# Optimization experiments

Hardware: AMD Instinct MI355X
Metric: run time of the kernel (lower is better)

The kernel has to match this reference:

```python
import jax, jax.numpy as jnp
import numpy as np

E, B, L, D = 3, 4, 1024, 768
DS = 64            # d_state
DI = 2 * D         # d_inner (expand=2)
DTR = 48           # dt_rank = ceil(D/16)
K = 4              # depthwise conv kernel size


def setup_inputs() -> dict:
    key = jax.random.key(0)
    ks = jax.random.split(key, 10)
    s = lambda i, shape, scale=0.02: (jax.random.normal(ks[i], shape, jnp.float32) * scale)
    A_log = jnp.broadcast_to(jnp.log(jnp.arange(1, DS + 1, dtype=jnp.float32)), (E, DI, DS))
    return {
        "base":   jax.random.normal(ks[0], (B, L, D), jnp.float32),
        "per_ch": jax.random.normal(ks[1], (E, B, L, D), jnp.float32),
        "alpha":  jnp.ones((E,), jnp.float32) / E,
        "ln_g":   jnp.ones((D,), jnp.float32),
        "ln_b":   jnp.zeros((D,), jnp.float32),
        "W_in":   s(2, (E, D, 2 * DI)),
        "conv_w": s(3, (E, DI, K), 0.1),
        "conv_b": jnp.zeros((E, DI), jnp.float32),
        "W_x":    s(4, (E, DI, DTR + 2 * DS)),
        "W_dt":   s(5, (E, DTR, DI), 0.05),
        "b_dt":   jnp.full((E, DI), -4.6, jnp.float32),  # softplus^-1(~0.01)
        "A_log":  A_log,
        "D_skip": jnp.ones((E, DI), jnp.float32),
        "W_out":  s(6, (E, DI, D)),
    }


def layer_norm(x, g, b, eps=1e-5):
    mu = jnp.mean(x, axis=-1, keepdims=True)
    var = jnp.mean(jnp.square(x - mu), axis=-1, keepdims=True)
    return (x - mu) * jax.lax.rsqrt(var + eps) * g + b


def mamba(x, W_in, conv_w, conv_b, W_x, W_dt, b_dt, A_log, D_skip, W_out):
    # x: [B, L, D]
    xz = x @ W_in                                   # [B, L, 2*DI]
    xp, z = jnp.split(xz, 2, axis=-1)               # each [B, L, DI]
    # causal depthwise conv along L
    xc = jnp.pad(xp, ((0, 0), (K - 1, 0), (0, 0)))
    xc = jax.lax.conv_general_dilated(
        jnp.swapaxes(xc, 1, 2),                     # [B, DI, L+K-1]
        conv_w[:, None, :],                         # [DI, 1, K]
        window_strides=(1,), padding='VALID',
        dimension_numbers=('NCH', 'OIH', 'NCH'),
        feature_group_count=DI)
    xc = jnp.swapaxes(xc, 1, 2) + conv_b            # [B, L, DI]
    xs = jax.nn.silu(xc)
    dbl = xs @ W_x                                  # [B, L, DTR+2*DS]
    dt, Bm, Cm = jnp.split(dbl, [DTR, DTR + DS], axis=-1)
    dt = jax.nn.softplus(dt @ W_dt + b_dt)          # [B, L, DI]
    A = -jnp.exp(A_log)                             # [DI, DS]

    def step(h, t):
        u_t, dt_t, B_t, C_t = t                     # [B,DI],[B,DI],[B,DS],[B,DS]
        dA = jnp.exp(dt_t[..., None] * A)           # [B, DI, DS]
        h = dA * h + (dt_t * u_t)[..., None] * B_t[:, None, :]
        y = jnp.einsum('bds,bs->bd', h, C_t)
        return h, y

    tm = lambda a: jnp.swapaxes(a, 0, 1)            # time-major
    h0 = jnp.zeros((x.shape[0], DI, DS), x.dtype)
    _, ys = jax.lax.scan(step, h0, (tm(xs), tm(dt), tm(Bm), tm(Cm)))
    y = jnp.swapaxes(ys, 0, 1) + xs * D_skip        # [B, L, DI]
    y = y * jax.nn.silu(z)
    return y @ W_out                                # [B, L, D]


def reference(base, per_ch, alpha, ln_g, ln_b, W_in, conv_w, conv_b, W_x,
              W_dt, b_dt, A_log, D_skip, W_out):
    w = jax.nn.softmax(alpha)                       # [E]
    xn = layer_norm(per_ch, ln_g, ln_b)             # shared LN on each channel
    outs = jax.vmap(mamba)(xn, W_in, conv_w, conv_b, W_x,
                           W_dt, b_dt, A_log, D_skip, W_out)  # [E, B, L, D]
    injection = jnp.einsum('e,ebld->bld', w, outs)
    return base + injection
```

## Files before the change

### kernel.cpp

```cpp
#include <hip/hip_runtime.h>
#include <hip/hip_bf16.h>

typedef __hip_bfloat16 bf16;
typedef unsigned short u16;
typedef __attribute__((ext_vector_type(8))) short s16x8;
typedef __attribute__((ext_vector_type(4))) short s16x4;
typedef __attribute__((ext_vector_type(4))) float f32x4;

#define EXP 3
#define BB  4
#define LL  1024
#define DD  768
#define DSN 64
#define DIN 1536
#define DTR 48
#define MM  4096

struct alignas(8)  bf16x4 { bf16 v[4]; };
struct alignas(16) bf16x8 { bf16 v[8]; };

__device__ __forceinline__ float siluf(float x) { return x / (1.f + __expf(-x)); }
__device__ __forceinline__ float softplusf(float x) { return (x > 15.f) ? x : log1pf(__expf(x)); }
__device__ __forceinline__ float bf2f(u16 h) { union { unsigned u; float f; } x; x.u = ((unsigned)h) << 16; return x.f; }

template <int CTRL>
__device__ __forceinline__ float ror_add(float x) {
  int y = __builtin_amdgcn_update_dpp(0, __float_as_int(x), CTRL, 0xf, 0xf, true);
  return x + __int_as_float(y);
}

__launch_bounds__(256)
__global__ void ln_apply_k(const float* __restrict__ pc, const float* __restrict__ lng,
                           const float* __restrict__ lnb, bf16* __restrict__ out) {
  int row  = blockIdx.x * 4 + (threadIdx.x >> 6);
  int lane = threadIdx.x & 63;
  const float* x = pc + (size_t)row * DD;
  float4 v[3];
  float s = 0.f, sq = 0.f;
#pragma unroll
  for (int i = 0; i < 3; i++) {
    v[i] = *(const float4*)(x + lane * 4 + i * 256);
    s  += v[i].x + v[i].y + v[i].z + v[i].w;
    sq += v[i].x * v[i].x + v[i].y * v[i].y + v[i].z * v[i].z + v[i].w * v[i].w;
  }
#pragma unroll
  for (int o = 1; o < 64; o <<= 1) { s += __shfl_xor(s, o); sq += __shfl_xor(sq, o); }
  float mu = s * (1.f / 768.f);
  float rs = rsqrtf(sq * (1.f / 768.f) - mu * mu + 1e-5f);
  bf16* op = out + (size_t)row * DD;
#pragma unroll
  for (int i = 0; i < 3; i++) {
    int col = lane * 4 + i * 256;
    float4 g4 = *(const float4*)(lng + col);
    float4 b4 = *(const float4*)(lnb + col);
    bf16x4 pk;
    pk.v[0] = (bf16)((v[i].x - mu) * rs * g4.x + b4.x);
    pk.v[1] = (bf16)((v[i].y - mu) * rs * g4.y + b4.y);
    pk.v[2] = (bf16)((v[i].z - mu) * rs * g4.z + b4.z);
    pk.v[3] = (bf16)((v[i].w - mu) * rs * g4.w + b4.w);
    *(bf16x4*)(op + col) = pk;
  }
}

__launch_bounds__(256)
__global__ void tcvt_k(const float* __restrict__ in, bf16* __restrict__ out,
                       int Ksrc, int ldin, int ldout,
                       size_t sIn, size_t sOut, int mode, const float* __restrict__ alphap) {
  __shared__ float tl[32][33];
  int z = blockIdx.z;
  const float* src = in + (size_t)z * sIn;
  bf16* dst = out + (size_t)z * sOut;
  int n0 = blockIdx.x * 32, k0 = blockIdx.y * 32;
  int tx = threadIdx.x, ty = threadIdx.y;
  int n = n0 + tx;
  int c = n; bool nv = true;
  if (mode == 1) {
    if (n < 48)       c = n;
    else if (n < 64)  nv = false;
    else if (n < 192) c = n - 16;
    else              nv = false;
  }
  float scale = 1.f;
  if (mode == 2) {
    float a0 = alphap[0], a1 = alphap[1], a2 = alphap[2];
    float mx = fmaxf(a0, fmaxf(a1, a2));
    float e0 = __expf(a0 - mx), e1 = __expf(a1 - mx), e2 = __expf(a2 - mx);
    scale = ((z == 0) ? e0 : (z == 1) ? e1 : e2) / (e0 + e1 + e2);
  }
#pragma unroll
  for (int i = 0; i < 32; i += 8) {
    int k = k0 + ty + i;
    float v = (nv && k < Ksrc) ? src[(size_t)k * ldin + c] : 0.f;
    tl[ty + i][tx] = v * scale;
  }
  __syncthreads();
#pragma unroll
  for (int i = 0; i < 32; i += 8) {
    dst[(size_t)(n0 + ty + i) * ldout + (k0 + tx)] = (bf16)tl[tx][ty + i];
  }
}

__launch_bounds__(256)
__global__ void conv_silu_k(const bf16* __restrict__ xp, const float* __restrict__ cw,
                            const float* __restrict__ cb, bf16* __restrict__ xs) {
  long i = ((long)blockIdx.x * 256 + threadIdx.x) * 8;
  int  c  = (int)(i % DIN);
  long rl = i / DIN;
  int  l  = (int)(rl & (LL - 1));
  int  e  = (int)(rl >> 12);
  const float* wp  = cw + (size_t)e * DIN * 4 + (size_t)c * 4;
  const float* cbp = cb + (size_t)e * DIN + c;
  float acc[8];
#pragma unroll
  for (int j = 0; j < 8; j++) acc[j] = cbp[j];
#pragma unroll
  for (int tap = 0; tap < 4; tap++) {
    if (l - 3 + tap >= 0) {
      s16x8 xv = *(const s16x8*)(const void*)(xp + (rl + tap - 3) * DIN + c);
#pragma unroll
      for (int j = 0; j < 8; j++)
        acc[j] = fmaf(bf2f((u16)xv[j]), wp[j * 4 + tap], acc[j]);
    }
  }
  bf16x8 pk;
#pragma unroll
  for (int j = 0; j < 8; j++) pk.v[j] = (bf16)siluf(acc[j]);
  *(bf16x8*)(xs + rl * DIN + c) = pk;
}

template<int MODE>
__launch_bounds__(256)
__global__ void mfma_gemm_k(const bf16* __restrict__ A, const bf16* __restrict__ Bt,
                            int Kdim, int lda,
                            size_t sA, size_t sB, size_t sO,
                            bf16* __restrict__ o0, bf16* __restrict__ o1,
                            const float* __restrict__ bias,
                            float* __restrict__ outp) {
  __shared__ short As[128 * 32];
  __shared__ short Bs[128 * 32];
  int z = blockIdx.z;
  A  += (size_t)z * sA;
  Bt += (size_t)z * sB;
  if (o0) o0 += (size_t)z * sO;
  if (o1) o1 += (size_t)z * sO;
  if constexpr (MODE == 1) outp += (size_t)z * (size_t)MM * 128;
  const float* bz = (MODE == 2) ? bias + (size_t)z * DIN : bias;

  int t = threadIdx.x;
  int l = t & 63, w = t >> 6;
  int wr = w >> 1, wc = w & 1;
  int n0 = blockIdx.x * 128, r0 = blockIdx.y * 128;

  int row = t >> 2, c3 = t & 3, col = c3 * 8;
  int plo = ((c3 & 1) ? 16 : 0) + ((c3 & 2) ? 4 : 0);
  int lrow = (l & 15) * 32 + (l >> 4) * 8;

  f32x4 acc[4][4] = {};

  for (int k0 = 0; k0 < Kdim; k0 += 32) {
    s16x8 va0 = *(const s16x8*)(const void*)(A  + (size_t)(r0 + row)      * lda  + k0 + col);
    s16x8 va1 = *(const s16x8*)(const void*)(A  + (size_t)(r0 + row + 64) * lda  + k0 + col);
    s16x8 vb0 = *(const s16x8*)(const void*)(Bt + (size_t)(n0 + row)      * Kdim + k0 + col);
    s16x8 vb1 = *(const s16x8*)(const void*)(Bt + (size_t)(n0 + row + 64) * Kdim + k0 + col);
    __syncthreads();
    *(s16x4*)(As + row * 32 + plo)          = __builtin_shufflevector(va0, va0, 0, 1, 2, 3);
    *(s16x4*)(As + row * 32 + plo + 8)      = __builtin_shufflevector(va0, va0, 4, 5, 6, 7);
    *(s16x4*)(As + (row + 64) * 32 + plo)     = __builtin_shufflevector(va1, va1, 0, 1, 2, 3);
    *(s16x4*)(As + (row + 64) * 32 + plo + 8) = __builtin_shufflevector(va1, va1, 4, 5, 6, 7);
    *(s16x4*)(Bs + row * 32 + plo)          = __builtin_shufflevector(vb0, vb0, 0, 1, 2, 3);
    *(s16x4*)(Bs + row * 32 + plo + 8)      = __builtin_shufflevector(vb0, vb0, 4, 5, 6, 7);
    *(s16x4*)(Bs + (row + 64) * 32 + plo)     = __builtin_shufflevector(vb1, vb1, 0, 1, 2, 3);
    *(s16x4*)(Bs + (row + 64) * 32 + plo + 8) = __builtin_shufflevector(vb1, vb1, 4, 5, 6, 7);
    __syncthreads();
    s16x8 af[4], bfv[4];
#pragma unroll
    for (int m = 0; m < 4; m++) af[m]  = *(const s16x8*)(As + (wr * 64 + m * 16) * 32 + lrow);
#pragma unroll
    for (int n = 0; n < 4; n++) bfv[n] = *(const s16x8*)(Bs + (wc * 64 + n * 16) * 32 + lrow);
#pragma unroll
    for (int m = 0; m < 4; m++)
#pragma unroll
      for (int n = 0; n < 4; n++)
        acc[m][n] = __builtin_amdgcn_mfma_f32_16x16x32_bf16(af[m], bfv[n], acc[m][n], 0, 0, 0);
  }

  int rb = r0 + wr * 64 + ((l >> 4) << 2);
  int cb = n0 + wc * 64 + (l & 15);
#pragma unroll
  for (int m = 0; m < 4; m++)
#pragma unroll
    for (int n = 0; n < 4; n++)
#pragma unroll
      for (int r = 0; r < 4; r++) {
        int gr = rb + m * 16 + r;
        int gc = cb + n * 16;
        float v = acc[m][n][r];
        if constexpr (MODE == 0) {
          if (n0 < DIN) o0[(size_t)gr * DIN + gc] = (bf16)v;
          else          o1[(size_t)gr * DIN + (gc - DIN)] = (bf16)siluf(v);
        } else if constexpr (MODE == 1) {
          if (gc < 64)       o0[(size_t)gr * 64 + gc] = (bf16)v;
          else if (gc < 192) outp[(size_t)gr * 128 + (gc - 64)] = v;
        } else if constexpr (MODE == 2) {
          o0[(size_t)gr * DIN + gc] = (bf16)softplusf(v + bz[gc]);
        } else {
          atomicAdd(&outp[(size_t)gr * DD + gc], v);
        }
      }
}

__launch_bounds__(256)
__global__ void copy4_k(const float* __restrict__ s, float* __restrict__ d, int n4) {
  int i = blockIdx.x * 256 + threadIdx.x;
  if (i < n4) ((float4*)d)[i] = ((const float4*)s)[i];
}

__launch_bounds__(256)
__global__ void scan_k(const bf16* __restrict__ dtb, bf16* __restrict__ xsb,
                       const bf16* __restrict__ gb, const float* __restrict__ dbl,
                       const float* __restrict__ A_log, const float* __restrict__ Dsk) {
  int gt = blockIdx.x * 256 + threadIdx.x;
  int sg = gt & 15;
  int cidx = gt >> 4;
  int d  = cidx % DIN;
  int eb = cidx / DIN;
  int e  = eb >> 2;

  float4 Ar = *(const float4*)(A_log + ((size_t)e * DIN + d) * DSN + sg * 4);
  const float LOG2E = 1.44269504088896f;
  float4 A2;
  A2.x = -__expf(Ar.x) * LOG2E;
  A2.y = -__expf(Ar.y) * LOG2E;
  A2.z = -__expf(Ar.z) * LOG2E;
  A2.w = -__expf(Ar.w) * LOG2E;
  float4 h = {0.f, 0.f, 0.f, 0.f};
  float dskip = Dsk[(size_t)e * DIN + d];

  unsigned idx  = (unsigned)eb * (LL * DIN) + (unsigned)d;
  unsigned bofs = (unsigned)eb * (LL * 128) + (unsigned)(sg * 4);

  float dtv = (float)dtb[idx];
  float u   = (float)xsb[idx];
  float gv  = (float)gb[idx];
  float4 Bv = *(const float4*)(dbl + bofs);
  float4 Cv = *(const float4*)(dbl + bofs + 64);

#pragma unroll 4
  for (int l = 0; l < LL; ++l) {
    unsigned idxn = idx + DIN;
    unsigned bofn = bofs + 128;
    float dtn = (float)dtb[idxn];
    float un  = (float)xsb[idxn];
    float gn  = (float)gb[idxn];
    float4 Bn = *(const float4*)(dbl + bofn);
    float4 Cn = *(const float4*)(dbl + bofn + 64);

    float du = dtv * u;
    float4 dA;
    dA.x = __builtin_amdgcn_exp2f(dtv * A2.x);
    dA.y = __builtin_amdgcn_exp2f(dtv * A2.y);
    dA.z = __builtin_amdgcn_exp2f(dtv * A2.z);
    dA.w = __builtin_amdgcn_exp2f(dtv * A2.w);
    h.x = fmaf(dA.x, h.x, du * Bv.x);
    h.y = fmaf(dA.y, h.y, du * Bv.y);
    h.z = fmaf(dA.z, h.z, du * Bv.z);
    h.w = fmaf(dA.w, h.w, du * Bv.w);
    float p = fmaf(h.x, Cv.x, fmaf(h.y, Cv.y, fmaf(h.z, Cv.z, h.w * Cv.w)));
    p = ror_add<0x128>(p);
    p = ror_add<0x124>(p);
    p = ror_add<0x122>(p);
    p = ror_add<0x121>(p);
    if (sg == 0) {
      xsb[idx] = (bf16)(fmaf(u, dskip, p) * gv);
    }
    idx = idxn; bofs = bofn;
    dtv = dtn; u = un; gv = gn; Bv = Bn; Cv = Cn;
  }
}

extern "C" void kernel_launch(void* const* d_in, const int* in_sizes, int n_in,
                              void* d_out, int out_size, void* d_ws, size_t ws_size,
                              hipStream_t stream) {
  const float* base   = (const float*)d_in[0];
  const float* per_ch = (const float*)d_in[1];
  const float* alpha  = (const float*)d_in[2];
  const float* ln_g   = (const float*)d_in[3];
  const float* ln_b   = (const float*)d_in[4];
  const float* W_in   = (const float*)d_in[5];
  const float* conv_w = (const float*)d_in[6];
  const float* conv_b = (const float*)d_in[7];
  const float* W_x    = (const float*)d_in[8];
  const float* W_dt   = (const float*)d_in[9];
  const float* b_dt   = (const float*)d_in[10];
  const float* A_log  = (const float*)d_in[11];
  const float* D_skip = (const float*)d_in[12];
  const float* W_out  = (const float*)d_in[13];
  float* out = (float*)d_out;
  (void)in_sizes; (void)n_in; (void)out_size; (void)ws_size;

  char* ws = (char*)d_ws;
  const size_t R = (size_t)EXP * MM * DIN * 2;
  bf16* Abf   = (bf16*)ws;
  bf16* xsws  = (bf16*)ws;
  bf16* gws   = (bf16*)(ws + R);
  bf16* dtws  = (bf16*)(ws + 2 * R);
  char* R4    = ws + 3 * R;
  bf16*  WinT  = (bf16*)R4;
  bf16*  WoutT = (bf16*)R4;
  float* dblf  = (float*)(R4 + 7077888);
  bf16* WxT   = (bf16*)(ws + 3 * R + 14155776);
  bf16* WdtT  = (bf16*)(ws + 3 * R + 14155776 + 2359296);
  bf16* dblp  = (bf16*)(ws + 3 * R + 14155776 + 2359296 + 589824);

  dim3 blk2(32, 8);

  ln_apply_k<<<EXP * BB * LL / 4, 256, 0, stream>>>(per_ch, ln_g, ln_b, Abf);
  tcvt_k<<<dim3(96, 24, EXP), blk2, 0, stream>>>(W_in, WinT, 768, 3072, 768,
        (size_t)768 * 3072, (size_t)3072 * 768, 0, nullptr);
  tcvt_k<<<dim3(8, 48, EXP), blk2, 0, stream>>>(W_x, WxT, 1536, 176, 1536,
        (size_t)1536 * 176, (size_t)256 * 1536, 1, nullptr);
  tcvt_k<<<dim3(48, 2, EXP), blk2, 0, stream>>>(W_dt, WdtT, 48, 1536, 64,
        (size_t)48 * 1536, (size_t)1536 * 64, 0, nullptr);

  mfma_gemm_k<0><<<dim3(24, 32, EXP), 256, 0, stream>>>(Abf, WinT, 768, DD,
        (size_t)MM * DD, (size_t)3072 * 768, (size_t)MM * DIN,
        dtws, gws, nullptr, nullptr);

  tcvt_k<<<dim3(24, 48, EXP), blk2, 0, stream>>>(W_out, WoutT, 1536, 768, 1536,
        (size_t)1536 * 768, (size_t)768 * 1536, 2, alpha);

  conv_silu_k<<<EXP * BB * LL * DIN / 8 / 256, 256, 0, stream>>>(dtws, conv_w, conv_b, xsws);

  mfma_gemm_k<1><<<dim3(2, 32, EXP), 256, 0, stream>>>(xsws, WxT, 1536, DIN,
        (size_t)MM * DIN, (size_t)256 * 1536, (size_t)MM * 64,
        dblp, nullptr, nullptr, dblf);

  mfma_gemm_k<2><<<dim3(12, 32, EXP), 256, 0, stream>>>(dblp, WdtT, 64, 64,
        (size_t)MM * 64, (size_t)1536 * 64, (size_t)MM * DIN,
        dtws, nullptr, b_dt, nullptr);

  copy4_k<<<MM * DD / 4 / 256, 256, 0, stream>>>(base, out, MM * DD / 4);
  scan_k<<<EXP * BB * DIN * 16 / 256, 256, 0, stream>>>(dtws, xsws, gws, dblf, A_log, D_skip);
  mfma_gemm_k<3><<<dim3(6, 32, EXP), 256, 0, stream>>>(xsws, WoutT, 1536, DIN,
        (size_t)MM * DIN, (size_t)768 * 1536, 0,
        nullptr, nullptr, nullptr, out);
}
```

Before: 898.3 us.

## Store dt and B/C time-major-transposed so scan loads contiguous vectors per channel

The dt projection GEMM now computes the transposed product so dt is stored as [E, DI, B*L], and the x-projection GEMM writes B/C as [E, 128, B*L] with vector stores. The scan reads four timesteps of dt in one 8-byte load and four timesteps of B/C per float4, then processes four steps per loop iteration. This replaces strided per-step loads of dt and B/C with contiguous vector loads and adds more prefetching per iteration. In exchange the MODE 1 epilogue performs transposed stores, and the scan holds more registers, which may lower occupancy.

```diff
diff --git a/kernel.cpp b/kernel.cpp
--- a/kernel.cpp
+++ b/kernel.cpp
@@ -143,7 +143,7 @@
   Bt += (size_t)z * sB;
   if (o0) o0 += (size_t)z * sO;
   if (o1) o1 += (size_t)z * sO;
-  if constexpr (MODE == 1) outp += (size_t)z * (size_t)MM * 128;
+  if constexpr (MODE == 1) outp += (size_t)z * (size_t)128 * MM;
   const float* bz = (MODE == 2) ? bias + (size_t)z * DIN : bias;
 
   int t = threadIdx.x;
@@ -186,27 +186,42 @@
 
   int rb = r0 + wr * 64 + ((l >> 4) << 2);
   int cb = n0 + wc * 64 + (l & 15);
-#pragma unroll
-  for (int m = 0; m < 4; m++)
-#pragma unroll
-    for (int n = 0; n < 4; n++)
-#pragma unroll
-      for (int r = 0; r < 4; r++) {
-        int gr = rb + m * 16 + r;
-        int gc = cb + n * 16;
-        float v = acc[m][n][r];
-        if constexpr (MODE == 0) {
-          if (n0 < DIN) o0[(size_t)gr * DIN + gc] = (bf16)v;
-          else          o1[(size_t)gr * DIN + (gc - DIN)] = (bf16)siluf(v);
-        } else if constexpr (MODE == 1) {
-          if (gc < 64)       o0[(size_t)gr * 64 + gc] = (bf16)v;
-          else if (gc < 192) outp[(size_t)gr * 128 + (gc - 64)] = v;
-        } else if constexpr (MODE == 2) {
-          o0[(size_t)gr * DIN + gc] = (bf16)softplusf(v + bz[gc]);
-        } else {
-          atomicAdd(&outp[(size_t)gr * DD + gc], v);
+
+  if constexpr (MODE == 1) {
+#pragma unroll
+    for (int m = 0; m < 4; m++)
+#pragma unroll
+      for (int n = 0; n < 4; n++) {
+        int gr0 = rb + m * 16;
+        int gc  = cb + n * 16;
+        if (gc < 64) {
+#pragma unroll
+          for (int r = 0; r < 4; r++)
+            o0[(size_t)(gr0 + r) * 64 + gc] = (bf16)acc[m][n][r];
+        } else if (gc < 192) {
+          *(f32x4*)(outp + (size_t)(gc - 64) * MM + gr0) = acc[m][n];
         }
       }
+  } else {
+#pragma unroll
+    for (int m = 0; m < 4; m++)
+#pragma unroll
+      for (int n = 0; n < 4; n++)
+#pragma unroll
+        for (int r = 0; r < 4; r++) {
+          int gr = rb + m * 16 + r;
+          int gc = cb + n * 16;
+          float v = acc[m][n][r];
+          if constexpr (MODE == 0) {
+            if (n0 < DIN) o0[(size_t)gr * DIN + gc] = (bf16)v;
+            else          o1[(size_t)gr * DIN + (gc - DIN)] = (bf16)siluf(v);
+          } else if constexpr (MODE == 2) {
+            o0[(size_t)gr * MM + gc] = (bf16)softplusf(v + bz[gr]);
+          } else {
+            atomicAdd(&outp[(size_t)gr * DD + gc], v);
+          }
+        }
+  }
 }
 
 __launch_bounds__(256)
@@ -216,66 +231,89 @@
 }
 
 __launch_bounds__(256)
-__global__ void scan_k(const bf16* __restrict__ dtb, bf16* __restrict__ xsb,
-                       const bf16* __restrict__ gb, const float* __restrict__ dbl,
+__global__ void scan_k(const bf16* __restrict__ dtT, bf16* __restrict__ xsb,
+                       const bf16* __restrict__ gb, const float* __restrict__ bcT,
                        const float* __restrict__ A_log, const float* __restrict__ Dsk) {
   int gt = blockIdx.x * 256 + threadIdx.x;
   int sg = gt & 15;
   int cidx = gt >> 4;
   int d  = cidx % DIN;
   int eb = cidx / DIN;
-  int e  = eb >> 2;
+  int e  = eb >> 2, b = eb & 3;
 
   float4 Ar = *(const float4*)(A_log + ((size_t)e * DIN + d) * DSN + sg * 4);
   const float LOG2E = 1.44269504088896f;
-  float4 A2;
-  A2.x = -__expf(Ar.x) * LOG2E;
-  A2.y = -__expf(Ar.y) * LOG2E;
-  A2.z = -__expf(Ar.z) * LOG2E;
-  A2.w = -__expf(Ar.w) * LOG2E;
-  float4 h = {0.f, 0.f, 0.f, 0.f};
+  float A2x = -__expf(Ar.x) * LOG2E;
+  float A2y = -__expf(Ar.y) * LOG2E;
+  float A2z = -__expf(Ar.z) * LOG2E;
+  float A2w = -__expf(Ar.w) * LOG2E;
   float dskip = Dsk[(size_t)e * DIN + d];
 
-  unsigned idx  = (unsigned)eb * (LL * DIN) + (unsigned)d;
-  unsigned bofs = (unsigned)eb * (LL * 128) + (unsigned)(sg * 4);
-
-  float dtv = (float)dtb[idx];
-  float u   = (float)xsb[idx];
-  float gv  = (float)gb[idx];
-  float4 Bv = *(const float4*)(dbl + bofs);
-  float4 Cv = *(const float4*)(dbl + bofs + 64);
-
-#pragma unroll 4
-  for (int l = 0; l < LL; ++l) {
-    unsigned idxn = idx + DIN;
-    unsigned bofn = bofs + 128;
-    float dtn = (float)dtb[idxn];
-    float un  = (float)xsb[idxn];
-    float gn  = (float)gb[idxn];
-    float4 Bn = *(const float4*)(dbl + bofn);
-    float4 Cn = *(const float4*)(dbl + bofn + 64);
-
-    float du = dtv * u;
-    float4 dA;
-    dA.x = __builtin_amdgcn_exp2f(dtv * A2.x);
-    dA.y = __builtin_amdgcn_exp2f(dtv * A2.y);
-    dA.z = __builtin_amdgcn_exp2f(dtv * A2.z);
-    dA.w = __builtin_amdgcn_exp2f(dtv * A2.w);
-    h.x = fmaf(dA.x, h.x, du * Bv.x);
-    h.y = fmaf(dA.y, h.y, du * Bv.y);
-    h.z = fmaf(dA.z, h.z, du * Bv.z);
-    h.w = fmaf(dA.w, h.w, du * Bv.w);
-    float p = fmaf(h.x, Cv.x, fmaf(h.y, Cv.y, fmaf(h.z, Cv.z, h.w * Cv.w)));
-    p = ror_add<0x128>(p);
-    p = ror_add<0x124>(p);
-    p = ror_add<0x122>(p);
-    p = ror_add<0x121>(p);
-    if (sg == 0) {
-      xsb[idx] = (bf16)(fmaf(u, dskip, p) * gv);
-    }
-    idx = idxn; bofs = bofn;
-    dtv = dtn; u = un; gv = gn; Bv = Bn; Cv = Cn;
-  }
+  const uint2*  dtp = (const uint2*)(dtT + (((size_t)e * DIN + d) << 12) + (b << 10));
+  const float4* Bq  = (const float4*)(bcT + (((size_t)e * 128 + sg * 4) << 12) + (b << 10));
+  unsigned idx = (unsigned)eb * (LL * DIN) + (unsigned)d;
+
+  float hx = 0.f, hy = 0.f, hz = 0.f, hw = 0.f;
+
+  uint2  dtu = dtp[0];
+  float4 B0 = Bq[0],     B1 = Bq[1024],  B2 = Bq[2048],  B3 = Bq[3072];
+  float4 C0 = Bq[65536], C1 = Bq[66560], C2 = Bq[67584], C3 = Bq[68608];
+  float u0 = (float)xsb[idx];
+  float u1 = (float)xsb[idx + DIN];
+  float u2 = (float)xsb[idx + 2 * DIN];
+  float u3 = (float)xsb[idx + 3 * DIN];
+  float g0 = (float)gb[idx];
+  float g1 = (float)gb[idx + DIN];
+  float g2 = (float)gb[idx + 2 * DIN];
+  float g3 = (float)gb[idx + 3 * DIN];
+
+#define SSTEP(DT, UU, GV, BX, BY, BZ, BW, CX, CY, CZ, CW, OFS)             \
+  {                                                                        \
+    float du = (DT) * (UU);                                                \
+    hx = fmaf(__builtin_amdgcn_exp2f((DT) * A2x), hx, du * (BX));          \
+    hy = fmaf(__builtin_amdgcn_exp2f((DT) * A2y), hy, du * (BY));          \
+    hz = fmaf(__builtin_amdgcn_exp2f((DT) * A2z), hz, du * (BZ));          \
+    hw = fmaf(__builtin_amdgcn_exp2f((DT) * A2w), hw, du * (BW));          \
+    float p = fmaf(hx, (CX), fmaf(hy, (CY), fmaf(hz, (CZ), hw * (CW))));   \
+    p = ror_add<0x128>(p);                                                 \
+    p = ror_add<0x124>(p);                                                 \
+    p = ror_add<0x122>(p);                                                 \
+    p = ror_add<0x121>(p);                                                 \
+    if (sg == 0) xsb[idx + (OFS)] = (bf16)(fmaf((UU), dskip, p) * (GV));   \
+  }
+
+  for (int t = 0; t < 256; ++t) {
+    uint2  dtn = dtp[t + 1];
+    float4 Bn0 = Bq[t + 1],     Bn1 = Bq[t + 1025],  Bn2 = Bq[t + 2049],  Bn3 = Bq[t + 3073];
+    float4 Cn0 = Bq[t + 65537], Cn1 = Bq[t + 66561], Cn2 = Bq[t + 67585], Cn3 = Bq[t + 68609];
+    unsigned idx4 = idx + 4 * DIN;
+    float un0 = (float)xsb[idx4];
+    float un1 = (float)xsb[idx4 + DIN];
+    float un2 = (float)xsb[idx4 + 2 * DIN];
+    float un3 = (float)xsb[idx4 + 3 * DIN];
+    float gn0 = (float)gb[idx4];
+    float gn1 = (float)gb[idx4 + DIN];
+    float gn2 = (float)gb[idx4 + 2 * DIN];
+    float gn3 = (float)gb[idx4 + 3 * DIN];
+
+    float dt0 = __uint_as_float(dtu.x << 16);
+    float dt1 = __uint_as_float(dtu.x & 0xffff0000u);
+    float dt2 = __uint_as_float(dtu.y << 16);
+    float dt3 = __uint_as_float(dtu.y & 0xffff0000u);
+
+    SSTEP(dt0, u0, g0, B0.x, B1.x, B2.x, B3.x, C0.x, C1.x, C2.x, C3.x, 0)
+    SSTEP(dt1, u1, g1, B0.y, B1.y, B2.y, B3.y, C0.y, C1.y, C2.y, C3.y, DIN)
+    SSTEP(dt2, u2, g2, B0.z, B1.z, B2.z, B3.z, C0.z, C1.z, C2.z, C3.z, 2 * DIN)
+    SSTEP(dt3, u3, g3, B0.w, B1.w, B2.w, B3.w, C0.w, C1.w, C2.w, C3.w, 3 * DIN)
+
+    idx = idx4;
+    dtu = dtn;
+    B0 = Bn0; B1 = Bn1; B2 = Bn2; B3 = Bn3;
+    C0 = Cn0; C1 = Cn1; C2 = Cn2; C3 = Cn3;
+    u0 = un0; u1 = un1; u2 = un2; u3 = un3;
+    g0 = gn0; g1 = gn1; g2 = gn2; g3 = gn3;
+  }
+#undef SSTEP
 }
 
 extern "C" void kernel_launch(void* const* d_in, const int* in_sizes, int n_in,
@@ -303,11 +341,12 @@
   bf16* Abf   = (bf16*)ws;
   bf16* xsws  = (bf16*)ws;
   bf16* gws   = (bf16*)(ws + R);
-  bf16* dtws  = (bf16*)(ws + 2 * R);
+  bf16* xpws  = (bf16*)(ws + 2 * R);
+  bf16* dtT   = (bf16*)(ws + 2 * R);
   char* R4    = ws + 3 * R;
   bf16*  WinT  = (bf16*)R4;
   bf16*  WoutT = (bf16*)R4;
-  float* dblf  = (float*)(R4 + 7077888);
+  float* bcT   = (float*)(R4 + 7077888);
   bf16* WxT   = (bf16*)(ws + 3 * R + 14155776);
   bf16* WdtT  = (bf16*)(ws + 3 * R + 14155776 + 2359296);
   bf16* dblp  = (bf16*)(ws + 3 * R + 14155776 + 2359296 + 589824);
@@ -324,23 +363,23 @@
 
   mfma_gemm_k<0><<<dim3(24, 32, EXP), 256, 0, stream>>>(Abf, WinT, 768, DD,
         (size_t)MM * DD, (size_t)3072 * 768, (size_t)MM * DIN,
-        dtws, gws, nullptr, nullptr);
+        xpws, gws, nullptr, nullptr);
 
   tcvt_k<<<dim3(24, 48, EXP), blk2, 0, stream>>>(W_out, WoutT, 1536, 768, 1536,
         (size_t)1536 * 768, (size_t)768 * 1536, 2, alpha);
 
-  conv_silu_k<<<EXP * BB * LL * DIN / 8 / 256, 256, 0, stream>>>(dtws, conv_w, conv_b, xsws);
+  conv_silu_k<<<EXP * BB * LL * DIN / 8 / 256, 256, 0, stream>>>(xpws, conv_w, conv_b, xsws);
 
   mfma_gemm_k<1><<<dim3(2, 32, EXP), 256, 0, stream>>>(xsws, WxT, 1536, DIN,
         (size_t)MM * DIN, (size_t)256 * 1536, (size_t)MM * 64,
-        dblp, nullptr, nullptr, dblf);
-
-  mfma_gemm_k<2><<<dim3(12, 32, EXP), 256, 0, stream>>>(dblp, WdtT, 64, 64,
-        (size_t)MM * 64, (size_t)1536 * 64, (size_t)MM * DIN,
-        dtws, nullptr, b_dt, nullptr);
+        dblp, nullptr, nullptr, bcT);
+
+  mfma_gemm_k<2><<<dim3(32, 12, EXP), 256, 0, stream>>>(WdtT, dblp, 64, 64,
+        (size_t)DIN * 64, (size_t)MM * 64, (size_t)DIN * MM,
+        dtT, nullptr, b_dt, nullptr);
 
   copy4_k<<<MM * DD / 4 / 256, 256, 0, stream>>>(base, out, MM * DD / 4);
-  scan_k<<<EXP * BB * DIN * 16 / 256, 256, 0, stream>>>(dtws, xsws, gws, dblf, A_log, D_skip);
+  scan_k<<<EXP * BB * DIN * 16 / 256, 256, 0, stream>>>(dtT, xsws, gws, bcT, A_log, D_skip);
   mfma_gemm_k<3><<<dim3(6, 32, EXP), 256, 0, stream>>>(xsws, WoutT, 1536, DIN,
         (size_t)MM * DIN, (size_t)768 * 1536, 0,
         nullptr, nullptr, nullptr, out);
```

After: 1.778 ms. 97.9% more time.

## Double-buffer MFMA GEMM tiles with direct global-to-LDS async loads

Applied to the files above, without the earlier changes.

The bf16 MFMA GEMM now stages A and B tiles straight from global memory into shared memory with `global_load_lds`, instead of loading into registers and shuffling stores. Shared memory is double-buffered so the next K-slice is fetched while MFMAs run on the current one, leaving one barrier per iteration. The LDS layout becomes two half-K planes, and fragments are rebuilt from two 4-element reads. This aims to hide global latency and drop register staging, at the cost of twice the LDS per block and reliance on correct wait handling for the async copies.

```diff
diff --git a/kernel.cpp b/kernel.cpp
--- a/kernel.cpp
+++ b/kernel.cpp
@@ -136,8 +136,8 @@
                             bf16* __restrict__ o0, bf16* __restrict__ o1,
                             const float* __restrict__ bias,
                             float* __restrict__ outp) {
-  __shared__ short As[128 * 32];
-  __shared__ short Bs[128 * 32];
+  __shared__ short As[2 * 128 * 32];
+  __shared__ short Bs[2 * 128 * 32];
   int z = blockIdx.z;
   A  += (size_t)z * sA;
   Bt += (size_t)z * sB;
@@ -151,38 +151,68 @@
   int wr = w >> 1, wc = w & 1;
   int n0 = blockIdx.x * 128, r0 = blockIdx.y * 128;
 
-  int row = t >> 2, c3 = t & 3, col = c3 * 8;
-  int plo = ((c3 & 1) ? 16 : 0) + ((c3 & 2) ? 4 : 0);
-  int lrow = (l & 15) * 32 + (l >> 4) * 8;
+  int s0  = w * 64 + l;
+  int rS  = (s0 >> 1) & 127;
+  int k8S = s0 & 1;
+  const bf16* srcA0 = A  + (size_t)(r0 + rS) * lda  + k8S * 8;
+  const bf16* srcA1 = srcA0 + 16;
+  const bf16* srcB0 = Bt + (size_t)(n0 + rS) * Kdim + k8S * 8;
+  const bf16* srcB1 = srcB0 + 16;
+  char* dA0 = (char*)As + (size_t)(w * 64) * 16;
+  char* dA1 = dA0 + 4096;
+  char* dB0 = (char*)Bs + (size_t)(w * 64) * 16;
+  char* dB1 = dB0 + 4096;
+
+#define STAGE(BUF, KOFF)                                                                     \
+  { int bo = (BUF) * 8192;                                                                   \
+    __builtin_amdgcn_global_load_lds(                                                        \
+        (const __attribute__((address_space(1))) void*)(srcA0 + (KOFF)),                     \
+        (__attribute__((address_space(3))) void*)(dA0 + bo), 16, 0, 0);                      \
+    __builtin_amdgcn_global_load_lds(                                                        \
+        (const __attribute__((address_space(1))) void*)(srcA1 + (KOFF)),                     \
+        (__attribute__((address_space(3))) void*)(dA1 + bo), 16, 0, 0);                      \
+    __builtin_amdgcn_global_load_lds(                                                        \
+        (const __attribute__((address_space(1))) void*)(srcB0 + (KOFF)),                     \
+        (__attribute__((address_space(3))) void*)(dB0 + bo), 16, 0, 0);                      \
+    __builtin_amdgcn_global_load_lds(                                                        \
+        (const __attribute__((address_space(1))) void*)(srcB1 + (KOFF)),                     \
+        (__attribute__((address_space(3))) void*)(dB1 + bo), 16, 0, 0); }
+
+  int rl15 = l & 15, hi = l >> 4;
+  int rdA = wr * 64 * 32 + rl15 * 32 + hi * 8;
+  int rdB = wc * 64 * 32 + rl15 * 32 + hi * 8;
 
   f32x4 acc[4][4] = {};
+  int buf = 0;
+  STAGE(0, 0)
+  __syncthreads();
 
   for (int k0 = 0; k0 < Kdim; k0 += 32) {
-    s16x8 va0 = *(const s16x8*)(const void*)(A  + (size_t)(r0 + row)      * lda  + k0 + col);
-    s16x8 va1 = *(const s16x8*)(const void*)(A  + (size_t)(r0 + row + 64) * lda  + k0 + col);
-    s16x8 vb0 = *(const s16x8*)(const void*)(Bt + (size_t)(n0 + row)      * Kdim + k0 + col);
-    s16x8 vb1 = *(const s16x8*)(const void*)(Bt + (size_t)(n0 + row + 64) * Kdim + k0 + col);
-    __syncthreads();
-    *(s16x4*)(As + row * 32 + plo)          = __builtin_shufflevector(va0, va0, 0, 1, 2, 3);
-    *(s16x4*)(As + row * 32 + plo + 8)      = __builtin_shufflevector(va0, va0, 4, 5, 6, 7);
-    *(s16x4*)(As + (row + 64) * 32 + plo)     = __builtin_shufflevector(va1, va1, 0, 1, 2, 3);
-    *(s16x4*)(As + (row + 64) * 32 + plo + 8) = __builtin_shufflevector(va1, va1, 4, 5, 6, 7);
-    *(s16x4*)(Bs + row * 32 + plo)          = __builtin_shufflevector(vb0, vb0, 0, 1, 2, 3);
-    *(s16x4*)(Bs + row * 32 + plo + 8)      = __builtin_shufflevector(vb0, vb0, 4, 5, 6, 7);
-    *(s16x4*)(Bs + (row + 64) * 32 + plo)     = __builtin_shufflevector(vb1, vb1, 0, 1, 2, 3);
-    *(s16x4*)(Bs + (row + 64) * 32 + plo + 8) = __builtin_shufflevector(vb1, vb1, 4, 5, 6, 7);
-    __syncthreads();
+    if (k0 + 32 < Kdim) STAGE(buf ^ 1, k0 + 32)
+    const char* pa = (const char*)As + buf * 8192 + rdA;
+    const char* pb = (const char*)Bs + buf * 8192 + rdB;
     s16x8 af[4], bfv[4];
 #pragma unroll
-    for (int m = 0; m < 4; m++) af[m]  = *(const s16x8*)(As + (wr * 64 + m * 16) * 32 + lrow);
-#pragma unroll
-    for (int n = 0; n < 4; n++) bfv[n] = *(const s16x8*)(Bs + (wc * 64 + n * 16) * 32 + lrow);
+    for (int m = 0; m < 4; m++) {
+      s16x4 lo  = *(const s16x4*)(pa + m * 512);
+      s16x4 hi4 = *(const s16x4*)(pa + m * 512 + 4096);
+      af[m] = __builtin_shufflevector(lo, hi4, 0, 1, 2, 3, 4, 5, 6, 7);
+    }
+#pragma unroll
+    for (int n = 0; n < 4; n++) {
+      s16x4 lo  = *(const s16x4*)(pb + n * 512);
+      s16x4 hi4 = *(const s16x4*)(pb + n * 512 + 4096);
+      bfv[n] = __builtin_shufflevector(lo, hi4, 0, 1, 2, 3, 4, 5, 6, 7);
+    }
 #pragma unroll
     for (int m = 0; m < 4; m++)
 #pragma unroll
       for (int n = 0; n < 4; n++)
         acc[m][n] = __builtin_amdgcn_mfma_f32_16x16x32_bf16(af[m], bfv[n], acc[m][n], 0, 0, 0);
-  }
+    __syncthreads();
+    buf ^= 1;
+  }
+#undef STAGE
 
   int rb = r0 + wr * 64 + ((l >> 4) << 2);
   int cb = n0 + wc * 64 + (l & 15);
```

Result: slower. 980.5 us (+9.1%).

## Split selective scan into chunked local scans plus carry-fix pass

Applied to the files above, without the earlier changes.

Replaces the sequential per-channel scan over the full sequence with a two-pass chunked scan. The first pass runs 4 chunks of 256 steps in parallel from a zero state, with 16 states per thread and a 4-lane reduction. It stores each chunk's end state in bf16 (in the output buffer as scratch) together with the summed dt. The second pass rebuilds the incoming carry from earlier chunks and adds its decayed contribution to y for chunks 1 to 3. This shortens the serial dependency chain and regroups the work per thread, at the cost of redundant exp work, extra memory traffic, and bf16 rounding of the carried state.

```diff
diff --git a/kernel.cpp b/kernel.cpp
--- a/kernel.cpp
+++ b/kernel.cpp
@@ -15,6 +15,9 @@
 #define DIN 1536
 #define DTR 48
 #define MM  4096
+#define NCH 18432
+#define NC  4
+#define CL  256
 
 struct alignas(8)  bf16x4 { bf16 v[4]; };
 struct alignas(16) bf16x8 { bf16 v[8]; };
@@ -24,7 +27,7 @@
 __device__ __forceinline__ float bf2f(u16 h) { union { unsigned u; float f; } x; x.u = ((unsigned)h) << 16; return x.f; }
 
 template <int CTRL>
-__device__ __forceinline__ float ror_add(float x) {
+__device__ __forceinline__ float dpp_add(float x) {
   int y = __builtin_amdgcn_update_dpp(0, __float_as_int(x), CTRL, 0xf, 0xf, true);
   return x + __int_as_float(y);
 }
@@ -216,65 +219,147 @@
 }
 
 __launch_bounds__(256)
-__global__ void scan_k(const bf16* __restrict__ dtb, bf16* __restrict__ xsb,
-                       const bf16* __restrict__ gb, const float* __restrict__ dbl,
-                       const float* __restrict__ A_log, const float* __restrict__ Dsk) {
+__global__ void scan_local_k(const bf16* __restrict__ dtb, bf16* __restrict__ xsb,
+                             const bf16* __restrict__ gb, const float* __restrict__ dblf,
+                             const float* __restrict__ A_log, const float* __restrict__ Dsk,
+                             bf16* __restrict__ hf, float* __restrict__ Ssum) {
   int gt = blockIdx.x * 256 + threadIdx.x;
-  int sg = gt & 15;
-  int cidx = gt >> 4;
-  int d  = cidx % DIN;
-  int eb = cidx / DIN;
+  int sg2  = gt & 3;
+  int rest = gt >> 2;
+  int ch    = rest % NCH;
+  int chunk = rest / NCH;
+  int d  = ch % DIN;
+  int eb = ch / DIN;
   int e  = eb >> 2;
 
-  float4 Ar = *(const float4*)(A_log + ((size_t)e * DIN + d) * DSN + sg * 4);
   const float LOG2E = 1.44269504088896f;
-  float4 A2;
-  A2.x = -__expf(Ar.x) * LOG2E;
-  A2.y = -__expf(Ar.y) * LOG2E;
-  A2.z = -__expf(Ar.z) * LOG2E;
-  A2.w = -__expf(Ar.w) * LOG2E;
-  float4 h = {0.f, 0.f, 0.f, 0.f};
+  float A2[16], h[16];
+  const float4* Ap = (const float4*)(A_log + ((size_t)e * DIN + d) * DSN + sg2 * 16);
+#pragma unroll
+  for (int i = 0; i < 4; i++) {
+    float4 a = Ap[i];
+    A2[4 * i + 0] = -__expf(a.x) * LOG2E;
+    A2[4 * i + 1] = -__expf(a.y) * LOG2E;
+    A2[4 * i + 2] = -__expf(a.z) * LOG2E;
+    A2[4 * i + 3] = -__expf(a.w) * LOG2E;
+    h[4 * i] = h[4 * i + 1] = h[4 * i + 2] = h[4 * i + 3] = 0.f;
+  }
   float dskip = Dsk[(size_t)e * DIN + d];
 
-  unsigned idx  = (unsigned)eb * (LL * DIN) + (unsigned)d;
-  unsigned bofs = (unsigned)eb * (LL * 128) + (unsigned)(sg * 4);
-
-  float dtv = (float)dtb[idx];
-  float u   = (float)xsb[idx];
-  float gv  = (float)gb[idx];
-  float4 Bv = *(const float4*)(dbl + bofs);
-  float4 Cv = *(const float4*)(dbl + bofs + 64);
-
-#pragma unroll 4
-  for (int l = 0; l < LL; ++l) {
-    unsigned idxn = idx + DIN;
-    unsigned bofn = bofs + 128;
-    float dtn = (float)dtb[idxn];
-    float un  = (float)xsb[idxn];
-    float gn  = (float)gb[idxn];
-    float4 Bn = *(const float4*)(dbl + bofn);
-    float4 Cn = *(const float4*)(dbl + bofn + 64);
-
+  int l0 = chunk * CL;
+  unsigned idx = (unsigned)eb * (LL * DIN) + (unsigned)(l0 * DIN) + (unsigned)d;
+  const float* bp = dblf + ((size_t)eb * LL + l0) * 128 + sg2 * 16;
+
+  float S = 0.f;
+  float u = (float)xsb[idx];
+
+  for (int t = 0; t < CL; ++t) {
+    float dtv = (float)dtb[idx];
+    float gv  = (float)gb[idx];
+    float un  = (float)xsb[idx + DIN];
+    float Bf[16], Cf[16];
+    *(float4*)&Bf[0]  = *(const float4*)(bp);
+    *(float4*)&Bf[4]  = *(const float4*)(bp + 4);
+    *(float4*)&Bf[8]  = *(const float4*)(bp + 8);
+    *(float4*)&Bf[12] = *(const float4*)(bp + 12);
+    *(float4*)&Cf[0]  = *(const float4*)(bp + 64);
+    *(float4*)&Cf[4]  = *(const float4*)(bp + 68);
+    *(float4*)&Cf[8]  = *(const float4*)(bp + 72);
+    *(float4*)&Cf[12] = *(const float4*)(bp + 76);
+
+    S += dtv;
     float du = dtv * u;
-    float4 dA;
-    dA.x = __builtin_amdgcn_exp2f(dtv * A2.x);
-    dA.y = __builtin_amdgcn_exp2f(dtv * A2.y);
-    dA.z = __builtin_amdgcn_exp2f(dtv * A2.z);
-    dA.w = __builtin_amdgcn_exp2f(dtv * A2.w);
-    h.x = fmaf(dA.x, h.x, du * Bv.x);
-    h.y = fmaf(dA.y, h.y, du * Bv.y);
-    h.z = fmaf(dA.z, h.z, du * Bv.z);
-    h.w = fmaf(dA.w, h.w, du * Bv.w);
-    float p = fmaf(h.x, Cv.x, fmaf(h.y, Cv.y, fmaf(h.z, Cv.z, h.w * Cv.w)));
-    p = ror_add<0x128>(p);
-    p = ror_add<0x124>(p);
-    p = ror_add<0x122>(p);
-    p = ror_add<0x121>(p);
-    if (sg == 0) {
+    float p = 0.f;
+#pragma unroll
+    for (int s = 0; s < 16; ++s) {
+      float dA = __builtin_amdgcn_exp2f(dtv * A2[s]);
+      h[s] = fmaf(dA, h[s], du * Bf[s]);
+      p = fmaf(h[s], Cf[s], p);
+    }
+    p = dpp_add<0xB1>(p);
+    p = dpp_add<0x4E>(p);
+    if (sg2 == 0) {
       xsb[idx] = (bf16)(fmaf(u, dskip, p) * gv);
     }
-    idx = idxn; bofs = bofn;
-    dtv = dtn; u = un; gv = gn; Bv = Bn; Cv = Cn;
+    idx += DIN; bp += 128; u = un;
+  }
+
+  if (chunk < NC - 1) {
+    bf16* hp = hf + (((size_t)chunk * NCH + ch) << 6) + sg2 * 16;
+    bf16x8 p0, p1;
+#pragma unroll
+    for (int j = 0; j < 8; j++) { p0.v[j] = (bf16)h[j]; p1.v[j] = (bf16)h[8 + j]; }
+    *(bf16x8*)hp       = p0;
+    *(bf16x8*)(hp + 8) = p1;
+    if (sg2 == 0) Ssum[chunk * NCH + ch] = S;
+  }
+}
+
+__launch_bounds__(256)
+__global__ void scan_fix_k(const bf16* __restrict__ dtb, bf16* __restrict__ xsb,
+                           const bf16* __restrict__ gb, const float* __restrict__ dblf,
+                           const float* __restrict__ A_log,
+                           const bf16* __restrict__ hf, const float* __restrict__ Ssum) {
+  int gt = blockIdx.x * 256 + threadIdx.x;
+  int sg2  = gt & 3;
+  int rest = gt >> 2;
+  int ch = rest % NCH;
+  int cf = 1 + rest / NCH;
+  int d  = ch % DIN;
+  int eb = ch / DIN;
+  int e  = eb >> 2;
+
+  const float LOG2E = 1.44269504088896f;
+  float A2[16];
+  const float4* Ap = (const float4*)(A_log + ((size_t)e * DIN + d) * DSN + sg2 * 16);
+#pragma unroll
+  for (int i = 0; i < 4; i++) {
+    float4 a = Ap[i];
+    A2[4 * i + 0] = -__expf(a.x) * LOG2E;
+    A2[4 * i + 1] = -__expf(a.y) * LOG2E;
+    A2[4 * i + 2] = -__expf(a.z) * LOG2E;
+    A2[4 * i + 3] = -__expf(a.w) * LOG2E;
+  }
+
+  float G[16];
+  {
+    const bf16* hp = hf + ((size_t)ch << 6) + sg2 * 16;
+#pragma unroll
+    for (int s = 0; s < 16; ++s) G[s] = (float)hp[s];
+  }
+  for (int j = 1; j < cf; ++j) {
+    float Sj = Ssum[j * NCH + ch];
+    const bf16* hp = hf + (((size_t)j * NCH + ch) << 6) + sg2 * 16;
+#pragma unroll
+    for (int s = 0; s < 16; ++s)
+      G[s] = fmaf(__builtin_amdgcn_exp2f(A2[s] * Sj), G[s], (float)hp[s]);
+  }
+
+  int l0 = cf * CL;
+  unsigned idx = (unsigned)eb * (LL * DIN) + (unsigned)(l0 * DIN) + (unsigned)d;
+  const float* bp = dblf + ((size_t)eb * LL + l0) * 128 + sg2 * 16;
+
+  for (int t = 0; t < CL; ++t) {
+    float dtv = (float)dtb[idx];
+    float Cf[16];
+    *(float4*)&Cf[0]  = *(const float4*)(bp + 64);
+    *(float4*)&Cf[4]  = *(const float4*)(bp + 68);
+    *(float4*)&Cf[8]  = *(const float4*)(bp + 72);
+    *(float4*)&Cf[12] = *(const float4*)(bp + 76);
+    float p = 0.f;
+#pragma unroll
+    for (int s = 0; s < 16; ++s) {
+      G[s] *= __builtin_amdgcn_exp2f(dtv * A2[s]);
+      p = fmaf(G[s], Cf[s], p);
+    }
+    p = dpp_add<0xB1>(p);
+    p = dpp_add<0x4E>(p);
+    if (sg2 == 0) {
+      float gv = (float)gb[idx];
+      float y  = (float)xsb[idx];
+      xsb[idx] = (bf16)fmaf(p, gv, y);
+    }
+    idx += DIN; bp += 128;
   }
 }
 
@@ -308,9 +393,11 @@
   bf16*  WinT  = (bf16*)R4;
   bf16*  WoutT = (bf16*)R4;
   float* dblf  = (float*)(R4 + 7077888);
+  float* Ssum  = (float*)(R4 + 13369344);
   bf16* WxT   = (bf16*)(ws + 3 * R + 14155776);
   bf16* WdtT  = (bf16*)(ws + 3 * R + 14155776 + 2359296);
   bf16* dblp  = (bf16*)(ws + 3 * R + 14155776 + 2359296 + 589824);
+  bf16* hf    = (bf16*)d_out;
 
   dim3 blk2(32, 8);
 
@@ -339,8 +426,12 @@
         (size_t)MM * 64, (size_t)1536 * 64, (size_t)MM * DIN,
         dtws, nullptr, b_dt, nullptr);
 
+  scan_local_k<<<NCH * 4 * NC / 256, 256, 0, stream>>>(
+      dtws, xsws, gws, dblf, A_log, D_skip, hf, Ssum);
+  scan_fix_k<<<NCH * 4 * (NC - 1) / 256, 256, 0, stream>>>(
+      dtws, xsws, gws, dblf, A_log, hf, Ssum);
+
   copy4_k<<<MM * DD / 4 / 256, 256, 0, stream>>>(base, out, MM * DD / 4);
-  scan_k<<<EXP * BB * DIN * 16 / 256, 256, 0, stream>>>(dtws, xsws, gws, dblf, A_log, D_skip);
   mfma_gemm_k<3><<<dim3(6, 32, EXP), 256, 0, stream>>>(xsws, WoutT, 1536, DIN,
         (size_t)MM * DIN, (size_t)768 * 1536, 0,
         nullptr, nullptr, nullptr, out);
```

Measured after the change: 1.326 ms. +47.6%, slower.
